# Kernel tuning notes

Hardware: AMD Instinct MI355X
Metric: run time of the kernel (lower is better)

## Reference

```python
import jax, jax.numpy as jnp
import numpy as np

TEMPERATURE = 1.0


def setup_inputs() -> dict:
    key = jax.random.key(0)
    k1, k2, k3, k4, k5 = jax.random.split(key, 5)
    B, D, Da, Dv = 8192, 128, 64, 64
    return {
        "a_features": jax.random.normal(k1, (B, D), dtype=jnp.float32),
        "v_features": jax.random.normal(k2, (B, D), dtype=jnp.float32),
        "audio_only_indices": jax.random.randint(k3, (Da,), 0, D, dtype=jnp.int64),
        "image_only_indices": jax.random.randint(k4, (Dv,), 0, D, dtype=jnp.int64),
        "labels": jax.random.randint(k5, (B,), 0, 10, dtype=jnp.int64),
    }


def reference(a_features, v_features, audio_only_indices, image_only_indices, labels):
    # Gather modality-specific feature subspaces: [B, Da] / [B, Dv]
    audio_only = a_features[:, audio_only_indices]          # a-features, audio dims
    image_audio_only = v_features[:, audio_only_indices]    # v-features, audio dims
    image_only = v_features[:, image_only_indices]          # v-features, image dims
    audio_image_only = a_features[:, image_only_indices]    # a-features, image dims

    # Per original: the dot-product partner is detached (stop_gradient).
    # v_loss_i = -log( exp(<v_i, a_i>/T) / sum_j exp(<v_i, a_j>/T) )
    #          = logsumexp_j(S_v[i, j]) - S_v[i, i]
    S_v = jnp.matmul(image_audio_only,
                     jax.lax.stop_gradient(audio_only).T) / TEMPERATURE  # [B, B]
    S_a = jnp.matmul(audio_image_only,
                     jax.lax.stop_gradient(image_only).T) / TEMPERATURE  # [B, B]

    v_loss = jnp.mean(jax.nn.logsumexp(S_v, axis=1) - jnp.diagonal(S_v))
    a_loss = jnp.mean(jax.nn.logsumexp(S_a, axis=1) - jnp.diagonal(S_a))
    return v_loss + a_loss
```

## Files before the change

kernel.cpp:

```cpp
#include <hip/hip_runtime.h>
#include <hip/hip_bf16.h>

typedef __attribute__((ext_vector_type(8))) short bf16x8;
typedef __attribute__((ext_vector_type(4))) float f32x4;
typedef __attribute__((ext_vector_type(16))) float f32x16;

#define BN 8192
#define DF 128
#define DG 64
static constexpr float L2E = 1.44269504088896340736f;
static constexpr float LN2 = 0.69314718055994530942f;

__device__ __forceinline__ size_t frag_off32(int row, int d) {
  int tile = row >> 5;
  int kk = d >> 4, khi = (d >> 3) & 1, c = d & 7;
  return (size_t)tile * 2048 + (size_t)kk * 512 +
         (size_t)(khi * 32 + (row & 31)) * 8 + c;
}

__global__ __launch_bounds__(256) void gather_k(
    const float* __restrict__ a, const float* __restrict__ v,
    const int* __restrict__ aidx, const int* __restrict__ iidx,
    __hip_bfloat16* __restrict__ Xv, __hip_bfloat16* __restrict__ Ya,
    __hip_bfloat16* __restrict__ Xa, __hip_bfloat16* __restrict__ Yv,
    float* __restrict__ diag, float* __restrict__ rowsum,
    float* __restrict__ out) {
  int tid = threadIdx.x;
  int gid = blockIdx.x * 256 + tid;
  if (gid < 2 * BN) rowsum[gid] = 0.f;
  if (gid == 0) out[0] = 0.f;

  int lane = tid & 63;
  int row  = blockIdx.x * 4 + (tid >> 6);
  int ka = aidx[lane];
  int ki = iidx[lane];

  float2 a2 = ((const float2*)(a + (size_t)row * DF))[lane];
  float2 v2 = ((const float2*)(v + (size_t)row * DF))[lane];

  float axa = __shfl(a2.x, ka >> 1), aya = __shfl(a2.y, ka >> 1);
  float vxa = __shfl(v2.x, ka >> 1), vya = __shfl(v2.y, ka >> 1);
  float axi = __shfl(a2.x, ki >> 1), ayi = __shfl(a2.y, ki >> 1);
  float vxi = __shfl(v2.x, ki >> 1), vyi = __shfl(v2.y, ki >> 1);
  float aa = (ka & 1) ? aya : axa;
  float va = (ka & 1) ? vya : vxa;
  float ai = (ki & 1) ? ayi : axi;
  float vi = (ki & 1) ? vyi : vxi;

  size_t fo = frag_off32(row, lane);
  Xv[fo] = __float2bfloat16(va * L2E);
  Ya[fo] = __float2bfloat16(aa);
  Xa[fo] = __float2bfloat16(ai * L2E);
  Yv[fo] = __float2bfloat16(vi);

  float dv = va * aa;
  float da = ai * vi;
#pragma unroll
  for (int off = 32; off >= 1; off >>= 1) {
    dv += __shfl_xor(dv, off);
    da += __shfl_xor(da, off);
  }
  if (lane == 0) {
    diag[row]      = dv;
    diag[BN + row] = da;
  }
}

__global__ __launch_bounds__(256, 4) void lse_main(
    const unsigned short* __restrict__ Xv, const unsigned short* __restrict__ Ya,
    const unsigned short* __restrict__ Xa, const unsigned short* __restrict__ Yv,
    float* __restrict__ rowsum) {
  const unsigned short* X;
  const unsigned short* Y;
  float* rs;
  if (blockIdx.z == 0) { X = Xv; Y = Ya; rs = rowsum; }
  else                 { X = Xa; Y = Yv; rs = rowsum + BN; }

  int tid  = threadIdx.x;
  int lane = tid & 63;
  int row0 = blockIdx.x * 128 + (tid >> 6) * 32;

  const unsigned short* ap =
      X + (size_t)(row0 >> 5) * 2048 + (size_t)lane * 8;
  bf16x8 a[4];
#pragma unroll
  for (int kk = 0; kk < 4; ++kk) a[kk] = *(const bf16x8*)(ap + kk * 512);

  const unsigned short* bbase =
      Y + (size_t)(blockIdx.y * 32) * 2048 + (size_t)lane * 8;

  const f32x16 zero16 = {};
  f32x16 part = {};
  bf16x8 b[4];

#define LOADB(T)                                                              \
  {                                                                           \
    const unsigned short* p = bbase + (size_t)(T) * 2048;                     \
    b[0] = *(const bf16x8*)p;                                                 \
    b[1] = *(const bf16x8*)(p + 512);                                         \
    b[2] = *(const bf16x8*)(p + 1024);                                        \
    b[3] = *(const bf16x8*)(p + 1536);                                        \
  }
#define CHAIN(DST)                                                            \
  {                                                                           \
    __builtin_amdgcn_s_setprio(1);                                            \
    DST = __builtin_amdgcn_mfma_f32_32x32x16_bf16(a[0], b[0], zero16, 0, 0, 0); \
    DST = __builtin_amdgcn_mfma_f32_32x32x16_bf16(a[1], b[1], DST, 0, 0, 0);  \
    DST = __builtin_amdgcn_mfma_f32_32x32x16_bf16(a[2], b[2], DST, 0, 0, 0);  \
    DST = __builtin_amdgcn_mfma_f32_32x32x16_bf16(a[3], b[3], DST, 0, 0, 0);  \
    __builtin_amdgcn_s_setprio(0);                                            \
  }
#define EXPACC(C)                                                             \
  {                                                                           \
    _Pragma("unroll") for (int r = 0; r < 16; ++r)                            \
        part[r] += __builtin_amdgcn_exp2f(C[r]);                              \
  }

  f32x16 c0, c1;
  LOADB(0)
  CHAIN(c0)
  LOADB(1)
  for (int i = 0; i < 15; ++i) {
    int t = 2 * i + 1;
    CHAIN(c1)
    LOADB(t + 1)
    EXPACC(c0)
    CHAIN(c0)
    LOADB(t + 2)
    EXPACC(c1)
  }
  CHAIN(c1)
  EXPACC(c0)
  EXPACC(c1)
#undef LOADB
#undef CHAIN
#undef EXPACC

#pragma unroll
  for (int off = 1; off < 32; off <<= 1) {
#pragma unroll
    for (int r = 0; r < 16; ++r)
      part[r] += __shfl_xor(part[r], off);
  }
  if ((lane & 31) == 0) {
    int hi = lane >> 5;
#pragma unroll
    for (int r = 0; r < 16; ++r) {
      int row = (r & 3) + 8 * (r >> 2) + 4 * hi;
      atomicAdd(&rs[row0 + row], part[r]);
    }
  }
}

__global__ __launch_bounds__(256) void finalize_k(
    const float* __restrict__ rowsum, const float* __restrict__ diag,
    float* __restrict__ out) {
  int i = blockIdx.x * 256 + threadIdx.x;
  float local = LN2 * __builtin_amdgcn_logf(rowsum[i]) - diag[i];
#pragma unroll
  for (int off = 32; off >= 1; off >>= 1) local += __shfl_xor(local, off);
  __shared__ float red[4];
  int wave = threadIdx.x >> 6;
  if ((threadIdx.x & 63) == 0) red[wave] = local;
  __syncthreads();
  if (threadIdx.x == 0) {
    float bs = red[0] + red[1] + red[2] + red[3];
    atomicAdd(out, bs * (1.f / (float)BN));
  }
}

extern "C" void kernel_launch(void* const* d_in, const int* in_sizes, int n_in,
                              void* d_out, int out_size, void* d_ws, size_t ws_size,
                              hipStream_t stream) {
  const float* a   = (const float*)d_in[0];
  const float* v   = (const float*)d_in[1];
  const int* aidx  = (const int*)d_in[2];
  const int* iidx  = (const int*)d_in[3];

  char* ws = (char*)d_ws;
  const size_t MB = 1024 * 1024;
  __hip_bfloat16* Xv = (__hip_bfloat16*)(ws + 0 * MB);
  __hip_bfloat16* Ya = (__hip_bfloat16*)(ws + 1 * MB);
  __hip_bfloat16* Xa = (__hip_bfloat16*)(ws + 2 * MB);
  __hip_bfloat16* Yv = (__hip_bfloat16*)(ws + 3 * MB);
  float* diag   = (float*)(ws + 4 * MB);
  float* rowsum = (float*)(ws + 4 * MB + 64 * 1024);

  gather_k<<<BN / 4, 256, 0, stream>>>(a, v, aidx, iidx, Xv, Ya, Xa, Yv,
                                       diag, rowsum, (float*)d_out);
  lse_main<<<dim3(BN / 128, 8, 2), 256, 0, stream>>>(
      (const unsigned short*)Xv, (const unsigned short*)Ya,
      (const unsigned short*)Xa, (const unsigned short*)Yv, rowsum);
  finalize_k<<<64, 256, 0, stream>>>(rowsum, diag, (float*)d_out);
}
```

Baseline: 93.73 us.

## Give each wave four A row tiles to reuse every loaded B tile

Each wave now holds four 32-row A tiles in registers and runs eight B column tiles against all of them, rather than one A tile against thirty-two B tiles. This cuts the global or L2 traffic for B per MFMA by four times and changes the grid to 16x32x2 blocks with launch bounds lowered to two blocks per SIMD. The cost is higher register pressure, with four partial accumulators and sixteen A fragments, and lower occupancy. The old two-chain software pipeline that overlapped exp with MFMA is replaced by a simpler double-buffered B load, and the atomics per row go from eight to thirty-two contributions.

```diff
diff --git a/kernel.cpp b/kernel.cpp
--- a/kernel.cpp
+++ b/kernel.cpp
@@ -66,7 +66,7 @@
   }
 }
 
-__global__ __launch_bounds__(256, 4) void lse_main(
+__global__ __launch_bounds__(256, 2) void lse_main(
     const unsigned short* __restrict__ Xv, const unsigned short* __restrict__ Ya,
     const unsigned short* __restrict__ Xa, const unsigned short* __restrict__ Yv,
     float* __restrict__ rowsum) {
@@ -78,77 +78,77 @@
 
   int tid  = threadIdx.x;
   int lane = tid & 63;
-  int row0 = blockIdx.x * 128 + (tid >> 6) * 32;
+  int wid  = tid >> 6;
+  int tile0 = blockIdx.x * 16 + wid * 4;
 
   const unsigned short* ap =
-      X + (size_t)(row0 >> 5) * 2048 + (size_t)lane * 8;
-  bf16x8 a[4];
+      X + (size_t)tile0 * 2048 + (size_t)lane * 8;
+  bf16x8 a[4][4];
 #pragma unroll
-  for (int kk = 0; kk < 4; ++kk) a[kk] = *(const bf16x8*)(ap + kk * 512);
+  for (int tt = 0; tt < 4; ++tt)
+#pragma unroll
+    for (int kk = 0; kk < 4; ++kk)
+      a[tt][kk] = *(const bf16x8*)(ap + tt * 2048 + kk * 512);
 
   const unsigned short* bbase =
-      Y + (size_t)(blockIdx.y * 32) * 2048 + (size_t)lane * 8;
+      Y + (size_t)(blockIdx.y * 8) * 2048 + (size_t)lane * 8;
 
   const f32x16 zero16 = {};
-  f32x16 part = {};
-  bf16x8 b[4];
+  f32x16 part[4] = {};
+  bf16x8 b[4], bn[4];
 
-#define LOADB(T)                                                              \
+#define LOADB(DST, T)                                                         \
   {                                                                           \
     const unsigned short* p = bbase + (size_t)(T) * 2048;                     \
-    b[0] = *(const bf16x8*)p;                                                 \
-    b[1] = *(const bf16x8*)(p + 512);                                         \
-    b[2] = *(const bf16x8*)(p + 1024);                                        \
-    b[3] = *(const bf16x8*)(p + 1536);                                        \
+    DST[0] = *(const bf16x8*)p;                                               \
+    DST[1] = *(const bf16x8*)(p + 512);                                       \
+    DST[2] = *(const bf16x8*)(p + 1024);                                      \
+    DST[3] = *(const bf16x8*)(p + 1536);                                      \
   }
-#define CHAIN(DST)                                                            \
+#define PROC(BB)                                                              \
   {                                                                           \
-    __builtin_amdgcn_s_setprio(1);                                            \
-    DST = __builtin_amdgcn_mfma_f32_32x32x16_bf16(a[0], b[0], zero16, 0, 0, 0); \
-    DST = __builtin_amdgcn_mfma_f32_32x32x16_bf16(a[1], b[1], DST, 0, 0, 0);  \
-    DST = __builtin_amdgcn_mfma_f32_32x32x16_bf16(a[2], b[2], DST, 0, 0, 0);  \
-    DST = __builtin_amdgcn_mfma_f32_32x32x16_bf16(a[3], b[3], DST, 0, 0, 0);  \
-    __builtin_amdgcn_s_setprio(0);                                            \
-  }
-#define EXPACC(C)                                                             \
-  {                                                                           \
-    _Pragma("unroll") for (int r = 0; r < 16; ++r)                            \
-        part[r] += __builtin_amdgcn_exp2f(C[r]);                              \
+    _Pragma("unroll") for (int tt = 0; tt < 4; ++tt) {                        \
+      f32x16 c;                                                               \
+      c = __builtin_amdgcn_mfma_f32_32x32x16_bf16(a[tt][0], BB[0], zero16, 0, 0, 0); \
+      c = __builtin_amdgcn_mfma_f32_32x32x16_bf16(a[tt][1], BB[1], c, 0, 0, 0); \
+      c = __builtin_amdgcn_mfma_f32_32x32x16_bf16(a[tt][2], BB[2], c, 0, 0, 0); \
+      c = __builtin_amdgcn_mfma_f32_32x32x16_bf16(a[tt][3], BB[3], c, 0, 0, 0); \
+      _Pragma("unroll") for (int r = 0; r < 16; ++r)                          \
+          part[tt][r] += __builtin_amdgcn_exp2f(c[r]);                        \
+    }                                                                         \
   }
 
-  f32x16 c0, c1;
-  LOADB(0)
-  CHAIN(c0)
-  LOADB(1)
-  for (int i = 0; i < 15; ++i) {
-    int t = 2 * i + 1;
-    CHAIN(c1)
-    LOADB(t + 1)
-    EXPACC(c0)
-    CHAIN(c0)
-    LOADB(t + 2)
-    EXPACC(c1)
+  LOADB(b, 0)
+#pragma unroll
+  for (int jj = 0; jj < 3; ++jj) {
+    LOADB(bn, 2 * jj + 1)
+    PROC(b)
+    LOADB(b, 2 * jj + 2)
+    PROC(bn)
   }
-  CHAIN(c1)
-  EXPACC(c0)
-  EXPACC(c1)
+  LOADB(bn, 7)
+  PROC(b)
+  PROC(bn)
 #undef LOADB
-#undef CHAIN
-#undef EXPACC
+#undef PROC
 
 #pragma unroll
   for (int off = 1; off < 32; off <<= 1) {
 #pragma unroll
-    for (int r = 0; r < 16; ++r)
-      part[r] += __shfl_xor(part[r], off);
+    for (int tt = 0; tt < 4; ++tt)
+#pragma unroll
+      for (int r = 0; r < 16; ++r)
+        part[tt][r] += __shfl_xor(part[tt][r], off);
   }
   if ((lane & 31) == 0) {
     int hi = lane >> 5;
 #pragma unroll
-    for (int r = 0; r < 16; ++r) {
-      int row = (r & 3) + 8 * (r >> 2) + 4 * hi;
-      atomicAdd(&rs[row0 + row], part[r]);
-    }
+    for (int tt = 0; tt < 4; ++tt)
+#pragma unroll
+      for (int r = 0; r < 16; ++r) {
+        int row = (r & 3) + 8 * (r >> 2) + 4 * hi;
+        atomicAdd(&rs[(tile0 + tt) * 32 + row], part[tt][r]);
+      }
   }
 }
 
@@ -188,7 +188,7 @@
 
   gather_k<<<BN / 4, 256, 0, stream>>>(a, v, aidx, iidx, Xv, Ya, Xa, Yv,
                                        diag, rowsum, (float*)d_out);
-  lse_main<<<dim3(BN / 128, 8, 2), 256, 0, stream>>>(
+  lse_main<<<dim3(BN / 512, 32, 2), 256, 0, stream>>>(
       (const unsigned short*)Xv, (const unsigned short*)Ya,
       (const unsigned short*)Xa, (const unsigned short*)Yv, rowsum);
   finalize_k<<<64, 256, 0, stream>>>(rowsum, diag, (float*)d_out);
```

Measured after the change: 103.1 us. 10.0% more time.
